# Kernel tuning notes

Hardware: AMD Instinct MI355X
Metric: run time of the kernel (lower is better)

Reference implementation:

```python
import jax, jax.numpy as jnp
import numpy as np

B, D, M = 32, 640, 1024
EPS = 1e-05


def setup_inputs() -> dict:
    key = jax.random.key(0)
    x = jax.random.normal(key, (B, D, M), dtype=jnp.float32)
    return {"x": x}


def _triu_flat_indices(d):
    iu, ju = np.triu_indices(d)
    return jnp.asarray(iu * d + ju, dtype=jnp.int32)


def reference(x):
    b, d, m = x.shape
    # Gram matrix: x @ x^T  -> [b, d, d]
    x_pow2 = jnp.einsum('bim,bjm->bij', x, x)
    # I_M @ (x_pow2 * I) + (x_pow2 * I) @ I_M - 2*x_pow2
    # (x_pow2 * I) is diagonal, so ones-matrix bmm = broadcast of the diagonal.
    diag = jnp.diagonal(x_pow2, axis1=1, axis2=2)  # [b, d]
    dcov = diag[:, None, :] + diag[:, :, None] - 2.0 * x_pow2
    dcov = jnp.maximum(dcov, 0.0)
    # temperature param is built in-forward: exp(log(1/(2*d*m))) = 1/(2*d*m)
    temperature = 1.0 / (2.0 * d * m)
    dcov = jnp.sqrt(temperature * dcov + EPS)
    # Double centering: dcov @ I_M = row sums broadcast; I_M @ dcov = col sums.
    row_mean = dcov.sum(axis=2, keepdims=True) / d          # [b, d, 1]
    col_mean = dcov.sum(axis=1, keepdims=True) / d          # [b, 1, d]
    tot_mean = dcov.sum(axis=(1, 2), keepdims=True) / (d * d)
    t = dcov - row_mean - col_mean + tot_mean               # [b, d, d]
    # Triuvec: gather upper-triangular entries (incl. diagonal)
    flat_idx = _triu_flat_indices(d)                         # [d*(d+1)//2]
    y = t.reshape(b, d * d)[:, flat_idx]
    return y
```

## Files before the change

### kernel.cpp

```cpp
#include <hip/hip_runtime.h>

#define D_DIM 640
#define M_DIM 1024
#define B_DIM 32
#define BK 32
#define OUT_ROW 205120

typedef __bf16 bf16x8 __attribute__((ext_vector_type(8)));
typedef float f32x4 __attribute__((ext_vector_type(4)));

__device__ __forceinline__ unsigned short f2bf(float f) {
    union { float f; unsigned int u; } c; c.f = f;
    unsigned int u = c.u;
    unsigned int r = (u + 0x7fffu + ((u >> 16) & 1u)) >> 16;
    return (unsigned short)r;
}

__device__ __forceinline__ float bf2f(unsigned short h) {
    union { unsigned int u; float f; } c; c.u = ((unsigned int)h) << 16;
    return c.f;
}

__device__ __forceinline__ void gload_lds16(const unsigned short* g, unsigned short* l) {
    __builtin_amdgcn_global_load_lds(
        (const __attribute__((address_space(1))) unsigned int*)g,
        (__attribute__((address_space(3))) unsigned int*)l,
        16, 0, 0);
}

__device__ __forceinline__ float block_reduce_256(float s) {
    #pragma unroll
    for (int off = 32; off > 0; off >>= 1) s += __shfl_down(s, off, 64);
    __shared__ float red[4];
    if ((threadIdx.x & 63) == 0) red[threadIdx.x >> 6] = s;
    __syncthreads();
    return red[0] + red[1] + red[2] + red[3];
}

__device__ __forceinline__ float block_reduce_512(float s) {
    #pragma unroll
    for (int off = 32; off > 0; off >>= 1) s += __shfl_down(s, off, 64);
    __shared__ float red[8];
    if ((threadIdx.x & 63) == 0) red[threadIdx.x >> 6] = s;
    __syncthreads();
    float t = 0.f;
    #pragma unroll
    for (int i = 0; i < 8; i++) t += red[i];
    return t;
}

__global__ void cast_diag_kernel(const float* __restrict__ x,
                                 unsigned short* __restrict__ xb,
                                 float* __restrict__ diag,
                                 float* __restrict__ rowsum,
                                 float* __restrict__ tot) {
    const size_t row = blockIdx.x;
    const int t = threadIdx.x;
    const float4 v = ((const float4*)(x + row * M_DIM))[t];
    float s = v.x * v.x + v.y * v.y + v.z * v.z + v.w * v.w;
    ushort4 o;
    o.x = f2bf(v.x); o.y = f2bf(v.y); o.z = f2bf(v.z); o.w = f2bf(v.w);
    ((ushort4*)(xb + row * M_DIM))[t] = o;
    float ssum = block_reduce_256(s);
    if (t == 0) { diag[row] = ssum; rowsum[row] = 0.f; }
    if (t == 1 && row < B_DIM) tot[row] = 0.f;
}

__global__ __launch_bounds__(512, 4)
void gemm_dcov_kernel(const unsigned short* __restrict__ xb,
                      const float* __restrict__ diag,
                      unsigned short* __restrict__ dcov,
                      float* __restrict__ rowsum,
                      float* __restrict__ tot) {
    __shared__ __align__(16) unsigned short smem[32768];

    const int id = blockIdx.x;
    const int bt = (id & 7) * 4 + ((id >> 3) & 3);
    int p = id >> 5;
    int it = 0, off = p;
    while (off >= 5 - it) { off -= 5 - it; ++it; }
    const int jt = it + off;
    const bool diagTile = (it == jt);

    const int tid = threadIdx.x;
    const int w = tid >> 6, l = tid & 63;
    const int wy = w >> 2, wx = w & 3;
    const int lm = l & 15, quad = l >> 4;

    const unsigned short* gA = xb + ((size_t)bt * D_DIM + it * 128) * M_DIM;
    const unsigned short* gB = xb + ((size_t)bt * D_DIM + jt * 128) * M_DIM;

    const int r0 = tid >> 2;
    const int cl = (((tid & 3) ^ ((tid >> 3) & 3)) << 3);
    const size_t aoff = (size_t)r0 * M_DIM + cl;
    const int ldst = tid * 8;

    auto issue = [&](int k, int ph) {
        unsigned short* sA = smem + ph * 8192;
        unsigned short* sB = sA + 4096;
        const int koff = k * BK;
        gload_lds16(gA + aoff + koff, sA + ldst);
        gload_lds16(gB + aoff + koff, sB + ldst);
    };

    f32x4 acc[4][2];
    const f32x4 zero = {0.f, 0.f, 0.f, 0.f};
    #pragma unroll
    for (int i = 0; i < 4; i++)
        #pragma unroll
        for (int j = 0; j < 2; j++) acc[i][j] = zero;

    const int sw = ((quad ^ ((lm >> 1) & 3)) << 3);

    issue(0, 0); issue(1, 1); issue(2, 2);

    int ph = 0;
    for (int k = 0; k < 32; ++k) {
        if (k < 30)       asm volatile("s_waitcnt vmcnt(4)" ::: "memory");
        else if (k == 30) asm volatile("s_waitcnt vmcnt(2)" ::: "memory");
        else              asm volatile("s_waitcnt vmcnt(0)" ::: "memory");
        asm volatile("s_barrier" ::: "memory");
        if (k + 3 < 32) issue(k + 3, (ph + 3) & 3);

        const unsigned short* sA = smem + ph * 8192;
        const unsigned short* sB = sA + 4096;
        bf16x8 af[4], bfr[2];
        #pragma unroll
        for (int mi = 0; mi < 4; mi++)
            af[mi] = *(const bf16x8*)&sA[(wy * 64 + mi * 16 + lm) * BK + sw];
        #pragma unroll
        for (int ni = 0; ni < 2; ni++)
            bfr[ni] = *(const bf16x8*)&sB[(wx * 32 + ni * 16 + lm) * BK + sw];

        #pragma unroll
        for (int mi = 0; mi < 4; mi++)
            #pragma unroll
            for (int ni = 0; ni < 2; ni++)
                acc[mi][ni] = __builtin_amdgcn_mfma_f32_16x16x32_bf16(
                    af[mi], bfr[ni], acc[mi][ni], 0, 0, 0);

        ph = (ph + 1) & 3;
    }

    float* sd = (float*)smem;
    if (tid < 128)      sd[tid] = diag[(size_t)bt * D_DIM + it * 128 + tid];
    else if (tid < 256) sd[tid] = diag[(size_t)bt * D_DIM + jt * 128 + (tid - 128)];
    __syncthreads();

    const float temp = 7.62939453125e-07f;
    unsigned short* dbase = dcov + (size_t)bt * D_DIM * D_DIM;
    float* rs = rowsum + (size_t)bt * D_DIM;
    float ts = 0.f;
    float cp[2] = {0.f, 0.f};

    #pragma unroll
    for (int mi = 0; mi < 4; mi++) {
        #pragma unroll
        for (int r = 0; r < 4; r++) {
            const int lrow = wy * 64 + mi * 16 + quad * 4 + r;
            const int grow = it * 128 + lrow;
            const float di = sd[lrow];
            float rp = 0.f;
            #pragma unroll
            for (int ni = 0; ni < 2; ni++) {
                const int lcol = wx * 32 + ni * 16 + lm;
                const int gcol = jt * 128 + lcol;
                const float dj = sd[128 + lcol];
                const float g = acc[mi][ni][r];
                const float v = sqrtf(fmaf(temp, fmaxf(di + dj - 2.f * g, 0.f), 1e-5f));
                dbase[(size_t)grow * D_DIM + gcol] = f2bf(v);
                rp += v;
                cp[ni] += v;
            }
            ts += rp;
            rp += __shfl_down(rp, 8, 16);
            rp += __shfl_down(rp, 4, 16);
            rp += __shfl_down(rp, 2, 16);
            rp += __shfl_down(rp, 1, 16);
            if (lm == 0) atomicAdd(&rs[grow], rp);
        }
    }
    if (!diagTile) {
        #pragma unroll
        for (int ni = 0; ni < 2; ni++) {
            float c = cp[ni];
            c += __shfl_down(c, 32);
            c += __shfl_down(c, 16);
            if (l < 16) atomicAdd(&rs[jt * 128 + wx * 32 + ni * 16 + lm], c);
        }
    }
    float bs = block_reduce_512(ts);
    if (tid == 0) atomicAdd(&tot[bt], diagTile ? bs : 2.f * bs);
}

__global__ void output_kernel(const unsigned short* __restrict__ dcov,
                              const float* __restrict__ rowsum,
                              const float* __restrict__ tot,
                              float* __restrict__ out) {
    const int b = blockIdx.x / D_DIM;
    const int i = blockIdx.x - b * D_DIM;
    const float inv_d = 1.f / (float)D_DIM;
    const float rmi = rowsum[(size_t)b * D_DIM + i] * inv_d;
    const float tm = tot[b] * (inv_d * inv_d);
    const unsigned short* drow = dcov + ((size_t)b * D_DIM + i) * D_DIM;
    const float* rs = rowsum + (size_t)b * D_DIM;
    float* orow = out + (size_t)b * OUT_ROW + (size_t)i * D_DIM - (size_t)i * (i - 1) / 2;
    for (int j = i + threadIdx.x; j < D_DIM; j += 256)
        orow[j - i] = bf2f(drow[j]) - rmi - rs[j] * inv_d + tm;
}

extern "C" void kernel_launch(void* const* d_in, const int* in_sizes, int n_in,
                              void* d_out, int out_size, void* d_ws, size_t ws_size,
                              hipStream_t stream) {
    const float* x = (const float*)d_in[0];
    float* out = (float*)d_out;

    char* ws = (char*)d_ws;
    unsigned short* xb = (unsigned short*)ws;
    size_t off = 41943040;
    float* diag = (float*)(ws + off);           off += 81920;
    unsigned short* dcov = (unsigned short*)(ws + off); off += 26214400;
    float* rowsum = (float*)(ws + off);         off += 81920;
    float* tot = (float*)(ws + off);            off += 256;

    cast_diag_kernel<<<dim3(B_DIM * D_DIM), 256, 0, stream>>>(x, xb, diag, rowsum, tot);
    gemm_dcov_kernel<<<dim3(480), 512, 0, stream>>>(xb, diag, dcov, rowsum, tot);
    output_kernel<<<dim3(B_DIM * D_DIM), 256, 0, stream>>>(dcov, rowsum, tot, out);
}
```

Baseline: 171.9 us.

## Load GEMM fragments directly from global into registers, dropping LDS staging

The GEMM main loop no longer stages A/B tiles through LDS with global_load_lds and barriers. Each lane now loads its MFMA fragments straight from global memory into registers, double-buffered across k-steps, and raises wave priority around the MFMA block. This removes LDS traffic and block-wide barriers, but every wave now fetches its own copy of shared rows with no LDS reuse, which puts more traffic on L1/L2 and uses more registers.

```diff
diff --git a/kernel.cpp b/kernel.cpp
--- a/kernel.cpp
+++ b/kernel.cpp
@@ -3,7 +3,6 @@
 #define D_DIM 640
 #define M_DIM 1024
 #define B_DIM 32
-#define BK 32
 #define OUT_ROW 205120
 
 typedef __bf16 bf16x8 __attribute__((ext_vector_type(8)));
@@ -19,13 +18,6 @@
 __device__ __forceinline__ float bf2f(unsigned short h) {
     union { unsigned int u; float f; } c; c.u = ((unsigned int)h) << 16;
     return c.f;
-}
-
-__device__ __forceinline__ void gload_lds16(const unsigned short* g, unsigned short* l) {
-    __builtin_amdgcn_global_load_lds(
-        (const __attribute__((address_space(1))) unsigned int*)g,
-        (__attribute__((address_space(3))) unsigned int*)l,
-        16, 0, 0);
 }
 
 __device__ __forceinline__ float block_reduce_256(float s) {
@@ -72,8 +64,6 @@
                       unsigned short* __restrict__ dcov,
                       float* __restrict__ rowsum,
                       float* __restrict__ tot) {
-    __shared__ __align__(16) unsigned short smem[32768];
-
     const int id = blockIdx.x;
     const int bt = (id & 7) * 4 + ((id >> 3) & 3);
     int p = id >> 5;
@@ -87,21 +77,8 @@
     const int wy = w >> 2, wx = w & 3;
     const int lm = l & 15, quad = l >> 4;
 
-    const unsigned short* gA = xb + ((size_t)bt * D_DIM + it * 128) * M_DIM;
-    const unsigned short* gB = xb + ((size_t)bt * D_DIM + jt * 128) * M_DIM;
-
-    const int r0 = tid >> 2;
-    const int cl = (((tid & 3) ^ ((tid >> 3) & 3)) << 3);
-    const size_t aoff = (size_t)r0 * M_DIM + cl;
-    const int ldst = tid * 8;
-
-    auto issue = [&](int k, int ph) {
-        unsigned short* sA = smem + ph * 8192;
-        unsigned short* sB = sA + 4096;
-        const int koff = k * BK;
-        gload_lds16(gA + aoff + koff, sA + ldst);
-        gload_lds16(gB + aoff + koff, sB + ldst);
-    };
+    const unsigned short* a0 = xb + ((size_t)bt * D_DIM + it * 128 + wy * 64 + lm) * M_DIM + quad * 8;
+    const unsigned short* b0 = xb + ((size_t)bt * D_DIM + jt * 128 + wx * 32 + lm) * M_DIM + quad * 8;
 
     f32x4 acc[4][2];
     const f32x4 zero = {0.f, 0.f, 0.f, 0.f};
@@ -110,39 +87,38 @@
         #pragma unroll
         for (int j = 0; j < 2; j++) acc[i][j] = zero;
 
-    const int sw = ((quad ^ ((lm >> 1) & 3)) << 3);
-
-    issue(0, 0); issue(1, 1); issue(2, 2);
-
-    int ph = 0;
-    for (int k = 0; k < 32; ++k) {
-        if (k < 30)       asm volatile("s_waitcnt vmcnt(4)" ::: "memory");
-        else if (k == 30) asm volatile("s_waitcnt vmcnt(2)" ::: "memory");
-        else              asm volatile("s_waitcnt vmcnt(0)" ::: "memory");
-        asm volatile("s_barrier" ::: "memory");
-        if (k + 3 < 32) issue(k + 3, (ph + 3) & 3);
-
-        const unsigned short* sA = smem + ph * 8192;
-        const unsigned short* sB = sA + 4096;
-        bf16x8 af[4], bfr[2];
+    bf16x8 aA[4], bA[2], aB[4], bB[2];
+
+    auto LD = [&](bf16x8* a, bf16x8* b, int k) {
+        const unsigned short* pa = a0 + k * 32;
+        const unsigned short* pb = b0 + k * 32;
         #pragma unroll
         for (int mi = 0; mi < 4; mi++)
-            af[mi] = *(const bf16x8*)&sA[(wy * 64 + mi * 16 + lm) * BK + sw];
+            a[mi] = *(const bf16x8*)(pa + (size_t)mi * 16 * M_DIM);
         #pragma unroll
         for (int ni = 0; ni < 2; ni++)
-            bfr[ni] = *(const bf16x8*)&sB[(wx * 32 + ni * 16 + lm) * BK + sw];
-
+            b[ni] = *(const bf16x8*)(pb + (size_t)ni * 16 * M_DIM);
+    };
+    auto MM = [&](bf16x8* a, bf16x8* b) {
+        __builtin_amdgcn_s_setprio(1);
         #pragma unroll
         for (int mi = 0; mi < 4; mi++)
             #pragma unroll
             for (int ni = 0; ni < 2; ni++)
                 acc[mi][ni] = __builtin_amdgcn_mfma_f32_16x16x32_bf16(
-                    af[mi], bfr[ni], acc[mi][ni], 0, 0, 0);
-
-        ph = (ph + 1) & 3;
+                    a[mi], b[ni], acc[mi][ni], 0, 0, 0);
+        __builtin_amdgcn_s_setprio(0);
+    };
+
+    LD(aA, bA, 0);
+    for (int k = 0; k < 32; k += 2) {
+        LD(aB, bB, k + 1);
+        MM(aA, bA);
+        if (k + 2 < 32) LD(aA, bA, k + 2);
+        MM(aB, bB);
     }
 
-    float* sd = (float*)smem;
+    __shared__ float sd[256];
     if (tid < 128)      sd[tid] = diag[(size_t)bt * D_DIM + it * 128 + tid];
     else if (tid < 256) sd[tid] = diag[(size_t)bt * D_DIM + jt * 128 + (tid - 128)];
     __syncthreads();
```

Result: slower. 231.3 us (+34.6%).

## Split GEMM tiles into 128x64 halves and pair triangle rows in output kernel

Applied to the files above, without the earlier changes.

The Gram/dcov kernel now gives each block a 128x64 sub-tile with 256 threads instead of a 128x128 tile with 512 threads. That doubles the grid to 960 blocks so the 256 CUs are filled more evenly, at the cost of reloading the A tile twice as often. The output kernel now pairs row i with row D-1-i in one block so every block writes a similar number of triangle elements, which removes the imbalance between long and short rows. Block count for the output kernel is halved.

```diff
diff --git a/kernel.cpp b/kernel.cpp
--- a/kernel.cpp
+++ b/kernel.cpp
@@ -3,7 +3,6 @@
 #define D_DIM 640
 #define M_DIM 1024
 #define B_DIM 32
-#define BK 32
 #define OUT_ROW 205120
 
 typedef __bf16 bf16x8 __attribute__((ext_vector_type(8)));
@@ -35,18 +34,6 @@
     if ((threadIdx.x & 63) == 0) red[threadIdx.x >> 6] = s;
     __syncthreads();
     return red[0] + red[1] + red[2] + red[3];
-}
-
-__device__ __forceinline__ float block_reduce_512(float s) {
-    #pragma unroll
-    for (int off = 32; off > 0; off >>= 1) s += __shfl_down(s, off, 64);
-    __shared__ float red[8];
-    if ((threadIdx.x & 63) == 0) red[threadIdx.x >> 6] = s;
-    __syncthreads();
-    float t = 0.f;
-    #pragma unroll
-    for (int i = 0; i < 8; i++) t += red[i];
-    return t;
 }
 
 __global__ void cast_diag_kernel(const float* __restrict__ x,
@@ -66,29 +53,31 @@
     if (t == 1 && row < B_DIM) tot[row] = 0.f;
 }
 
-__global__ __launch_bounds__(512, 4)
+__global__ __launch_bounds__(256, 3)
 void gemm_dcov_kernel(const unsigned short* __restrict__ xb,
                       const float* __restrict__ diag,
                       unsigned short* __restrict__ dcov,
                       float* __restrict__ rowsum,
                       float* __restrict__ tot) {
-    __shared__ __align__(16) unsigned short smem[32768];
+    __shared__ __align__(16) unsigned short smem[24576];
 
     const int id = blockIdx.x;
     const int bt = (id & 7) * 4 + ((id >> 3) & 3);
-    int p = id >> 5;
-    int it = 0, off = p;
+    const int rest = id >> 5;
+    const int jh = rest & 1;
+    int p2 = rest >> 1;
+    int it = 0, off = p2;
     while (off >= 5 - it) { off -= 5 - it; ++it; }
     const int jt = it + off;
     const bool diagTile = (it == jt);
 
     const int tid = threadIdx.x;
     const int w = tid >> 6, l = tid & 63;
-    const int wy = w >> 2, wx = w & 3;
+    const int wy = w >> 1, wx = w & 1;
     const int lm = l & 15, quad = l >> 4;
 
     const unsigned short* gA = xb + ((size_t)bt * D_DIM + it * 128) * M_DIM;
-    const unsigned short* gB = xb + ((size_t)bt * D_DIM + jt * 128) * M_DIM;
+    const unsigned short* gB = xb + ((size_t)bt * D_DIM + jt * 128 + jh * 64) * M_DIM;
 
     const int r0 = tid >> 2;
     const int cl = (((tid & 3) ^ ((tid >> 3) & 3)) << 3);
@@ -96,10 +85,11 @@
     const int ldst = tid * 8;
 
     auto issue = [&](int k, int ph) {
-        unsigned short* sA = smem + ph * 8192;
+        unsigned short* sA = smem + ph * 6144;
         unsigned short* sB = sA + 4096;
-        const int koff = k * BK;
+        const int koff = k * 32;
         gload_lds16(gA + aoff + koff, sA + ldst);
+        gload_lds16(gA + aoff + (size_t)64 * M_DIM + koff, sA + ldst + 2048);
         gload_lds16(gB + aoff + koff, sB + ldst);
     };
 
@@ -114,23 +104,22 @@
 
     issue(0, 0); issue(1, 1); issue(2, 2);
 
-    int ph = 0;
     for (int k = 0; k < 32; ++k) {
-        if (k < 30)       asm volatile("s_waitcnt vmcnt(4)" ::: "memory");
-        else if (k == 30) asm volatile("s_waitcnt vmcnt(2)" ::: "memory");
+        if (k < 30)       asm volatile("s_waitcnt vmcnt(6)" ::: "memory");
+        else if (k == 30) asm volatile("s_waitcnt vmcnt(3)" ::: "memory");
         else              asm volatile("s_waitcnt vmcnt(0)" ::: "memory");
         asm volatile("s_barrier" ::: "memory");
-        if (k + 3 < 32) issue(k + 3, (ph + 3) & 3);
-
-        const unsigned short* sA = smem + ph * 8192;
+        if (k + 3 < 32) issue(k + 3, (k + 3) & 3);
+
+        const unsigned short* sA = smem + (k & 3) * 6144;
         const unsigned short* sB = sA + 4096;
         bf16x8 af[4], bfr[2];
         #pragma unroll
         for (int mi = 0; mi < 4; mi++)
-            af[mi] = *(const bf16x8*)&sA[(wy * 64 + mi * 16 + lm) * BK + sw];
+            af[mi] = *(const bf16x8*)&sA[(wy * 64 + mi * 16 + lm) * 32 + sw];
         #pragma unroll
         for (int ni = 0; ni < 2; ni++)
-            bfr[ni] = *(const bf16x8*)&sB[(wx * 32 + ni * 16 + lm) * BK + sw];
+            bfr[ni] = *(const bf16x8*)&sB[(wx * 32 + ni * 16 + lm) * 32 + sw];
 
         #pragma unroll
         for (int mi = 0; mi < 4; mi++)
@@ -138,13 +127,11 @@
             for (int ni = 0; ni < 2; ni++)
                 acc[mi][ni] = __builtin_amdgcn_mfma_f32_16x16x32_bf16(
                     af[mi], bfr[ni], acc[mi][ni], 0, 0, 0);
-
-        ph = (ph + 1) & 3;
     }
 
     float* sd = (float*)smem;
     if (tid < 128)      sd[tid] = diag[(size_t)bt * D_DIM + it * 128 + tid];
-    else if (tid < 256) sd[tid] = diag[(size_t)bt * D_DIM + jt * 128 + (tid - 128)];
+    else if (tid < 192) sd[tid] = diag[(size_t)bt * D_DIM + jt * 128 + jh * 64 + (tid - 128)];
     __syncthreads();
 
     const float temp = 7.62939453125e-07f;
@@ -164,7 +151,7 @@
             #pragma unroll
             for (int ni = 0; ni < 2; ni++) {
                 const int lcol = wx * 32 + ni * 16 + lm;
-                const int gcol = jt * 128 + lcol;
+                const int gcol = jt * 128 + jh * 64 + lcol;
                 const float dj = sd[128 + lcol];
                 const float g = acc[mi][ni][r];
                 const float v = sqrtf(fmaf(temp, fmaxf(di + dj - 2.f * g, 0.f), 1e-5f));
@@ -186,10 +173,10 @@
             float c = cp[ni];
             c += __shfl_down(c, 32);
             c += __shfl_down(c, 16);
-            if (l < 16) atomicAdd(&rs[jt * 128 + wx * 32 + ni * 16 + lm], c);
+            if (l < 16) atomicAdd(&rs[jt * 128 + jh * 64 + wx * 32 + ni * 16 + lm], c);
         }
     }
-    float bs = block_reduce_512(ts);
+    float bs = block_reduce_256(ts);
     if (tid == 0) atomicAdd(&tot[bt], diagTile ? bs : 2.f * bs);
 }
 
@@ -197,16 +184,21 @@
                               const float* __restrict__ rowsum,
                               const float* __restrict__ tot,
                               float* __restrict__ out) {
-    const int b = blockIdx.x / D_DIM;
-    const int i = blockIdx.x - b * D_DIM;
+    const int b = blockIdx.x / 320;
+    const int q = blockIdx.x - b * 320;
     const float inv_d = 1.f / (float)D_DIM;
-    const float rmi = rowsum[(size_t)b * D_DIM + i] * inv_d;
     const float tm = tot[b] * (inv_d * inv_d);
-    const unsigned short* drow = dcov + ((size_t)b * D_DIM + i) * D_DIM;
     const float* rs = rowsum + (size_t)b * D_DIM;
-    float* orow = out + (size_t)b * OUT_ROW + (size_t)i * D_DIM - (size_t)i * (i - 1) / 2;
-    for (int j = i + threadIdx.x; j < D_DIM; j += 256)
-        orow[j - i] = bf2f(drow[j]) - rmi - rs[j] * inv_d + tm;
+
+    #pragma unroll
+    for (int half = 0; half < 2; half++) {
+        const int i = half ? (D_DIM - 1 - q) : q;
+        const float rmi = rs[i] * inv_d;
+        const unsigned short* drow = dcov + ((size_t)b * D_DIM + i) * D_DIM;
+        float* orow = out + (size_t)b * OUT_ROW + (size_t)i * D_DIM - (size_t)i * (i - 1) / 2;
+        for (int j = i + threadIdx.x; j < D_DIM; j += 256)
+            orow[j - i] = bf2f(drow[j]) - rmi - rs[j] * inv_d + tm;
+    }
 }
 
 extern "C" void kernel_launch(void* const* d_in, const int* in_sizes, int n_in,
@@ -224,6 +216,6 @@
     float* tot = (float*)(ws + off);            off += 256;
 
     cast_diag_kernel<<<dim3(B_DIM * D_DIM), 256, 0, stream>>>(x, xb, diag, rowsum, tot);
-    gemm_dcov_kernel<<<dim3(480), 512, 0, stream>>>(xb, diag, dcov, rowsum, tot);
-    output_kernel<<<dim3(B_DIM * D_DIM), 256, 0, stream>>>(dcov, rowsum, tot, out);
-}
+    gemm_dcov_kernel<<<dim3(960), 256, 0, stream>>>(xb, diag, dcov, rowsum, tot);
+    output_kernel<<<dim3(B_DIM * 320), 256, 0, stream>>>(dcov, rowsum, tot, out);
+}
```

Result: slower. 185.6 us (+8.0%).
